# Optimization experiments

Measured on AMD Instinct MI355X. Metric: run time of the kernel, lower is better.

Reference implementation:

```python
import jax, jax.numpy as jnp
import numpy as np

B, T, C, H, DH = 2, 2048, 768, 12, 64


def setup_inputs() -> dict:
    key = jax.random.key(0)
    k1, k2, k3 = jax.random.split(key, 3)
    x = jax.random.normal(k1, (B, T, C), dtype=jnp.float32)
    Wqkv = jax.random.normal(k2, (C, 3 * C), dtype=jnp.float32) * (C ** -0.5)
    Wout = jax.random.normal(k3, (C, C), dtype=jnp.float32) * (C ** -0.5)
    return {"x": x, "Wqkv": Wqkv, "Wout": Wout}


def reference(x, Wqkv, Wout):
    b, t, c = x.shape
    qkv = x @ Wqkv  # [B,T,3C]
    q, k, v = jnp.split(qkv, 3, axis=-1)
    # [B,T,C] -> [B,H,T,dh]
    q = q.reshape(b, t, H, DH).transpose(0, 2, 1, 3)
    k = k.reshape(b, t, H, DH).transpose(0, 2, 1, 3)
    v = v.reshape(b, t, H, DH).transpose(0, 2, 1, 3)
    scale = DH ** -0.5
    scores = jnp.einsum('bhqd,bhkd->bhqk', q, k) * scale  # [B,H,T,T]
    causal = jnp.tril(jnp.ones((t, t), dtype=bool))
    scores = jnp.where(causal, scores, -jnp.inf)
    weights = jax.nn.softmax(scores, axis=-1)
    # dropout p=0.0 -> identity
    out = jnp.einsum('bhqk,bhkd->bhqd', weights, v)  # [B,H,T,dh]
    out = out.transpose(0, 2, 1, 3).reshape(b, t, c)
    return out @ Wout
```

## Files before the change

### kernel.cpp

```cpp
#include <hip/hip_runtime.h>
#include <hip/hip_bf16.h>

#define Bn 2
#define Tn 2048
#define Cn 768
#define Hn 12
#define Dn 64
#define N3n 2304
#define Mn 4096

#define MASKVAL (-30000.f)
#define NIT_G 144
#define DEFER_THR 64.f
#define L2E8 0.1803368801111204f

typedef unsigned short u16;
typedef __attribute__((ext_vector_type(8))) unsigned short ushort8_t;
typedef __attribute__((ext_vector_type(8))) short bf16x8;
typedef __attribute__((ext_vector_type(4))) float f32x4;
typedef __attribute__((ext_vector_type(2))) unsigned int uint2v;
typedef __attribute__((address_space(1))) unsigned int* gas1_t;
typedef __attribute__((address_space(3))) unsigned int* las3_t;

__device__ __forceinline__ float bf2f(u16 u) {
  union { unsigned int i; float f; } v; v.i = ((unsigned int)u) << 16; return v.f;
}
__device__ __forceinline__ u16 f2bf(float f) {
  union { float f; unsigned int i; } v; v.f = f;
  return (u16)((v.i + 0x7fffu + ((v.i >> 16) & 1u)) >> 16);
}

#define E(qt, s0, s1, ck) (((qt) << 24) | ((s0) << 16) | ((s1) << 8) | (ck))
__constant__ unsigned int SCHED[48] = {
    E(31, 0, 8, 0), E(31, 8, 16, 1), E(30, 0, 8, 0), E(30, 8, 16, 1),
    E(29, 0, 8, 0), E(28, 0, 8, 0), E(15, 0, 8, 2), E(14, 0, 8, 2),
    E(29, 8, 15, 1), E(28, 8, 15, 1), E(27, 0, 7, 0), E(27, 7, 14, 1),
    E(26, 0, 7, 0), E(26, 7, 14, 1), E(25, 0, 7, 0), E(24, 0, 7, 0),
    E(13, 0, 7, 2), E(12, 0, 7, 2),
    E(25, 7, 13, 1), E(24, 7, 13, 1), E(23, 0, 6, 0), E(23, 6, 12, 1),
    E(22, 0, 6, 0), E(22, 6, 12, 1), E(21, 0, 6, 0), E(20, 0, 6, 0),
    E(11, 0, 6, 2), E(10, 0, 6, 2),
    E(21, 6, 11, 1), E(20, 6, 11, 1), E(19, 0, 5, 0), E(19, 5, 10, 1),
    E(18, 0, 5, 0), E(18, 5, 10, 1), E(17, 0, 5, 0), E(16, 0, 5, 0),
    E(9, 0, 5, 2), E(8, 0, 5, 2),
    E(17, 5, 9, 1), E(16, 5, 9, 1), E(7, 0, 4, 2), E(6, 0, 4, 2),
    E(5, 0, 3, 2), E(4, 0, 3, 2), E(3, 0, 2, 2), E(2, 0, 2, 2),
    E(1, 0, 1, 2), E(0, 0, 1, 2)};

__global__ __launch_bounds__(256) void prep_kernel(const float* __restrict__ x,
                                                   const float* __restrict__ Wqkv,
                                                   const float* __restrict__ Wout,
                                                   u16* __restrict__ xb,
                                                   u16* __restrict__ WqkvT,
                                                   u16* __restrict__ WoutT,
                                                   int* __restrict__ counter) {
  __shared__ u16 t[32][33];
  const int bx = blockIdx.x;
  const int tid = threadIdx.x;
  if (bx < 3072) {
    if (bx == 0 && tid < 8) counter[tid] = 0;
    const int i = (bx * 256 + tid) * 4;
    float4 v = *(const float4*)(x + i);
    ushort4 s;
    s.x = f2bf(v.x); s.y = f2bf(v.y); s.z = f2bf(v.z); s.w = f2bf(v.w);
    *(ushort4*)(xb + i) = s;
  } else {
    const int idx = bx - 3072;
    const int gx = idx % 96, gy = idx / 96;
    const bool isA = gx < (N3n / 32);
    const float* in = isA ? Wqkv : Wout;
    u16* out = isA ? WqkvT : WoutT;
    const int Cc = isA ? N3n : Cn;
    const int c0 = (isA ? gx : gx - N3n / 32) * 32;
    const int r0 = gy * 32;
    const int tx = tid & 31, ty = tid >> 5;
#pragma unroll
    for (int i = 0; i < 4; i++)
      t[ty * 4 + i][tx] = f2bf(in[(size_t)(r0 + ty * 4 + i) * Cc + c0 + tx]);
    __syncthreads();
#pragma unroll
    for (int i = 0; i < 4; i++)
      out[(size_t)(c0 + ty * 4 + i) * Cn + r0 + tx] = t[tx][ty * 4 + i];
  }
}

#define BK 64
#define GT_W (128 * BK)

template <int EPI>
__global__ __launch_bounds__(256) void mfma_gemm(const u16* __restrict__ A,
                                                 const u16* __restrict__ BT,
                                                 u16* __restrict__ Q,
                                                 u16* __restrict__ Kd,
                                                 u16* __restrict__ VT,
                                                 float* __restrict__ out) {
  __shared__ __align__(16) u16 Ash[2 * GT_W];
  __shared__ __align__(16) u16 Bsh[2 * GT_W];
  const int tid = threadIdx.x;
  const int wv = tid >> 6, lane = tid & 63;
  const int lo = lane & 15, quad = lane >> 4;
  const int lo7 = lo & 7;
  const int wm = wv & 1, wn = wv >> 1;

  const int nwg = gridDim.x * gridDim.y;
  const int cpx = nwg >> 3;
  const int lid = blockIdx.y * gridDim.x + blockIdx.x;
  const int swz = (lid & 7) * cpx + (lid >> 3);
  const int n0 = (swz % gridDim.x) * 128;
  const int m0 = (swz / gridDim.x) * 128;

  const int srow = lane >> 3;
  const int kcol = ((lane & 7) ^ srow) << 3;

  f32x4 acc[4][4];
#pragma unroll
  for (int i = 0; i < 4; i++)
#pragma unroll
    for (int j = 0; j < 4; j++) acc[i][j] = f32x4{0.f, 0.f, 0.f, 0.f};

  auto stage = [&](int k0, int buf) {
#pragma unroll
    for (int c = 0; c < 4; c++) {
      const int rb = (wv << 5) + (c << 3);
      const int gr = rb + srow;
      __builtin_amdgcn_global_load_lds(
          (gas1_t)(A + (size_t)(m0 + gr) * Cn + k0 + kcol),
          (las3_t)(&Ash[buf * GT_W + rb * BK]), 16, 0, 0);
      __builtin_amdgcn_global_load_lds(
          (gas1_t)(BT + (size_t)(n0 + gr) * Cn + k0 + kcol),
          (las3_t)(&Bsh[buf * GT_W + rb * BK]), 16, 0, 0);
    }
  };

  stage(0, 0);
  __syncthreads();

  int cur = 0;
  for (int k0 = 0; k0 < Cn; k0 += BK) {
    if (k0 + BK < Cn) stage(k0 + BK, cur ^ 1);

    const u16* Ab = &Ash[cur * GT_W];
    const u16* Bb = &Bsh[cur * GT_W];
    bf16x8 af[4][2], bfr[4][2];
#pragma unroll
    for (int t = 0; t < 4; t++) {
#pragma unroll
      for (int s = 0; s < 2; s++) {
        const int cc = ((s * 4 + quad) ^ lo7) << 3;
        af[t][s]  = *(const bf16x8*)&Ab[(wm * 64 + t * 16 + lo) * BK + cc];
        bfr[t][s] = *(const bf16x8*)&Bb[(wn * 64 + t * 16 + lo) * BK + cc];
      }
    }
#pragma unroll
    for (int mt = 0; mt < 4; mt++)
#pragma unroll
      for (int nt = 0; nt < 4; nt++) {
        acc[mt][nt] = __builtin_amdgcn_mfma_f32_16x16x32_bf16(af[mt][0], bfr[nt][0],
                                                              acc[mt][nt], 0, 0, 0);
        acc[mt][nt] = __builtin_amdgcn_mfma_f32_16x16x32_bf16(af[mt][1], bfr[nt][1],
                                                              acc[mt][nt], 0, 0, 0);
      }
    __syncthreads();
    cur ^= 1;
  }

  if (EPI == 0) {
    const int which = n0 / Cn;
    const int h = ((n0 % Cn) >> 6) + wn;
    const int bb = m0 >> 11;
    const int t_base = (m0 & (Tn - 1)) + wm * 64;
    if (which < 2) {
      u16* dst = ((which == 0) ? Q : Kd) + (size_t)(bb * Hn + h) * Tn * Dn;
#pragma unroll
      for (int mt = 0; mt < 4; mt++)
#pragma unroll
        for (int nt = 0; nt < 4; nt++)
#pragma unroll
          for (int r = 0; r < 4; r++) {
            const int t = t_base + mt * 16 + (quad << 2) + r;
            dst[(size_t)t * Dn + nt * 16 + lo] = f2bf(acc[mt][nt][r]);
          }
    } else {
      u16* dst = VT + (size_t)(bb * Hn + h) * Dn * Tn;
#pragma unroll
      for (int mt = 0; mt < 4; mt++)
#pragma unroll
        for (int nt = 0; nt < 4; nt++) {
          const int t = t_base + mt * 16 + (quad << 2);
          const int d = nt * 16 + lo;
          ushort4 st;
          st.x = f2bf(acc[mt][nt][0]); st.y = f2bf(acc[mt][nt][1]);
          st.z = f2bf(acc[mt][nt][2]); st.w = f2bf(acc[mt][nt][3]);
          *(ushort4*)&dst[(size_t)d * Tn + t] = st;
        }
    }
  } else {
#pragma unroll
    for (int mt = 0; mt < 4; mt++)
#pragma unroll
      for (int nt = 0; nt < 4; nt++)
#pragma unroll
        for (int r = 0; r < 4; r++) {
          const int m = m0 + wm * 64 + mt * 16 + (quad << 2) + r;
          out[(size_t)m * Cn + n0 + wn * 64 + nt * 16 + lo] = acc[mt][nt][r];
        }
  }
}

#define KT_W (128 * 64)
#define VH_W (64 * 64)

__global__ __launch_bounds__(256) void attn_kernel(const u16* __restrict__ Q,
                                                   const u16* __restrict__ K,
                                                   const u16* __restrict__ VT,
                                                   u16* __restrict__ O,
                                                   int* __restrict__ counter,
                                                   float* __restrict__ po,
                                                   float* __restrict__ pm,
                                                   float* __restrict__ pl) {
  __shared__ __align__(16) u16 Ksh[2 * KT_W];
  __shared__ __align__(16) u16 Vsh[4 * VH_W];
  int* sip = (int*)&Ksh[KT_W];

  const int tid = threadIdx.x;
  const int g = blockIdx.x & 7;
  const int wv = tid >> 6, lane = tid & 63;
  const int lo = lane & 15, quad = lane >> 4;
  const int lo7 = lo & 7;
  const int ck0 = (quad ^ lo7) << 3;
  const int ck1 = ck0 ^ 32;
  const int sr = tid >> 3;
  const int sc = (tid & 7) << 3;
  const int kcol = ((lane & 7) ^ (lane >> 3)) << 3;
  const int t7 = tid & 7;
  const int vb0 = (((t7 & 6) ^ (sr & 7)) << 3) + ((t7 & 1) << 2);
  const int vb1 = ((((t7 & 6) | 1) ^ (sr & 7)) << 3) + ((t7 & 1) << 2);

  for (;;) {
    if (tid == 0) *sip = atomicAdd(&counter[g], 1);
    __syncthreads();
    const int il = *sip;
    if (il >= NIT_G) return;

    const unsigned int e = SCHED[il / 3];
    const int qt = e >> 24, ck = e & 255;
    const int jstart = ((e >> 16) & 255) << 7;
    const int jend   = ((e >> 8) & 255) << 7;
    const int q0 = qt << 6;
    const int hb = g * 3 + il % 3;
    const int h = hb % 12, b = hb / 12;
    const size_t base = (size_t)(b * Hn + h) * Tn * Dn;
    const size_t vtb  = (size_t)(b * Hn + h) * Dn * Tn;
    const u16* Kg = K + base;

    const u16* qp = Q + base + (size_t)(q0 + (wv << 4) + lo) * Dn + (quad << 3);
    const bf16x8 aq0 = *(const bf16x8*)qp;
    const bf16x8 aq1 = *(const bf16x8*)(qp + 32);

    f32x4 o[4] = {f32x4{0,0,0,0}, f32x4{0,0,0,0}, f32x4{0,0,0,0}, f32x4{0,0,0,0}};
    float m1 = MASKVAL;
    float l1 = 0.f;

#pragma unroll
    for (int c = 0; c < 4; c++) {
      const int rb = (wv << 5) + (c << 3);
      __builtin_amdgcn_global_load_lds(
          (gas1_t)(Kg + (size_t)(jstart + rb + (lane >> 3)) * Dn + kcol),
          (las3_t)(&Ksh[rb * 64]), 16, 0, 0);
    }
#pragma unroll
    for (int hf = 0; hf < 2; hf++)
#pragma unroll
      for (int it = 0; it < 2; it++) {
        const int r = sr + it * 32;
        union { ushort8_t u; uint2v hh[2]; } vv;
        vv.u = *(const ushort8_t*)(VT + vtb + (size_t)r * Tn + jstart + hf * 64 + sc);
        *(uint2v*)&Vsh[hf * VH_W + r * 64 + vb0] = vv.hh[0];
        *(uint2v*)&Vsh[hf * VH_W + r * 64 + vb1] = vv.hh[1];
      }
    __syncthreads();

    int cur = 0;
    const int qg = q0 + (wv << 4) + lo;

    for (int j0 = jstart; j0 < jend; j0 += 128) {
      const bool hasnext = (j0 + 128 < jend);

      ushort8_t vr[4];
      if (hasnext) {
        const int nb = cur ^ 1;
#pragma unroll
        for (int c = 0; c < 4; c++) {
          const int rb = (wv << 5) + (c << 3);
          __builtin_amdgcn_global_load_lds(
              (gas1_t)(Kg + (size_t)(j0 + 128 + rb + (lane >> 3)) * Dn + kcol),
              (las3_t)(&Ksh[nb * KT_W + rb * 64]), 16, 0, 0);
        }
#pragma unroll
        for (int hf = 0; hf < 2; hf++)
#pragma unroll
          for (int it = 0; it < 2; it++) {
            const int r = sr + it * 32;
            vr[hf * 2 + it] =
                *(const ushort8_t*)(VT + vtb + (size_t)r * Tn + j0 + 128 + hf * 64 + sc);
          }
      }

      const u16* Kb_ = &Ksh[cur * KT_W];
      const u16* VbA = &Vsh[cur * 2 * VH_W];
      const u16* VbB = VbA + VH_W;

      f32x4 s[8];
      __builtin_amdgcn_s_setprio(1);
#pragma unroll
      for (int nt = 0; nt < 8; nt++) {
        const bf16x8 bk0 = *(const bf16x8*)(&Kb_[(nt * 16 + lo) * 64 + ck0]);
        const bf16x8 bk1 = *(const bf16x8*)(&Kb_[(nt * 16 + lo) * 64 + ck1]);
        f32x4 a = {0.f, 0.f, 0.f, 0.f};
        a = __builtin_amdgcn_mfma_f32_16x16x32_bf16(bk0, aq0, a, 0, 0, 0);
        a = __builtin_amdgcn_mfma_f32_16x16x32_bf16(bk1, aq1, a, 0, 0, 0);
        s[nt] = a;
      }
      __builtin_amdgcn_s_setprio(0);

      if (j0 + 128 > q0) {
#pragma unroll
        for (int nt = 0; nt < 8; nt++)
#pragma unroll
          for (int r = 0; r < 4; r++) {
            const int kvg = j0 + nt * 16 + (quad << 2) + r;
            if (kvg > qg) s[nt][r] = MASKVAL;
          }
      }

      float gm[8];
#pragma unroll
      for (int nt = 0; nt < 8; nt++)
        gm[nt] = fmaxf(fmaxf(s[nt][0], s[nt][1]), fmaxf(s[nt][2], s[nt][3]));
      const float pmax = fmaxf(fmaxf(fmaxf(gm[0], gm[1]), fmaxf(gm[2], gm[3])),
                               fmaxf(fmaxf(gm[4], gm[5]), fmaxf(gm[6], gm[7])));

      if (!__all(pmax <= m1 + DEFER_THR)) {
        float mr = fmaxf(pmax, __shfl_xor(pmax, 16));
        mr = fmaxf(mr, __shfl_xor(mr, 32));
        const float mnew = fmaxf(m1, mr);
        const float alpha = __builtin_amdgcn_exp2f(L2E8 * (m1 - mnew));
        m1 = mnew;
        l1 *= alpha;
        float ar[4];
#pragma unroll
        for (int r = 0; r < 4; r++) ar[r] = __shfl(alpha, (quad << 2) + r);
#pragma unroll
        for (int nt = 0; nt < 4; nt++)
#pragma unroll
          for (int r = 0; r < 4; r++) o[nt][r] *= ar[r];
      }

      const float mb2 = L2E8 * m1;
#pragma unroll
      for (int nt = 0; nt < 8; nt++)
#pragma unroll
        for (int r = 0; r < 4; r++)
          s[nt][r] = __builtin_amdgcn_exp2f(L2E8 * s[nt][r] - mb2);
      {
        float gs[8];
#pragma unroll
        for (int nt = 0; nt < 8; nt++)
          gs[nt] = (s[nt][0] + s[nt][1]) + (s[nt][2] + s[nt][3]);
        l1 += ((gs[0] + gs[1]) + (gs[2] + gs[3])) +
              ((gs[4] + gs[5]) + (gs[6] + gs[7]));
      }

      unsigned int A0, B0, A1, B1, A2, B2, A3, B3;
      union { unsigned int w[4]; bf16x8 v; } pa0u, pa1u, pa2u, pa3u;
      asm("v_cvt_pk_bf16_f32 %0, %1, %2" : "=v"(A0) : "v"(s[0][0]), "v"(s[0][1]));
      asm("v_cvt_pk_bf16_f32 %0, %1, %2" : "=v"(B0) : "v"(s[0][2]), "v"(s[0][3]));
      asm("v_cvt_pk_bf16_f32 %0, %1, %2" : "=v"(A1) : "v"(s[1][0]), "v"(s[1][1]));
      asm("v_cvt_pk_bf16_f32 %0, %1, %2" : "=v"(B1) : "v"(s[1][2]), "v"(s[1][3]));
      asm("v_cvt_pk_bf16_f32 %0, %1, %2" : "=v"(A2) : "v"(s[2][0]), "v"(s[2][1]));
      asm("v_cvt_pk_bf16_f32 %0, %1, %2" : "=v"(B2) : "v"(s[2][2]), "v"(s[2][3]));
      asm("v_cvt_pk_bf16_f32 %0, %1, %2" : "=v"(A3) : "v"(s[3][0]), "v"(s[3][1]));
      asm("v_cvt_pk_bf16_f32 %0, %1, %2" : "=v"(B3) : "v"(s[3][2]), "v"(s[3][3]));
      {
        const auto rA01 = __builtin_amdgcn_permlane32_swap(A0, A1, false, false);
        const auto rB01 = __builtin_amdgcn_permlane32_swap(B0, B1, false, false);
        const auto rA23 = __builtin_amdgcn_permlane32_swap(A2, A3, false, false);
        const auto rB23 = __builtin_amdgcn_permlane32_swap(B2, B3, false, false);
        pa0u.w[0] = rA01[0]; pa0u.w[1] = rB01[0];
        pa0u.w[2] = rA01[1]; pa0u.w[3] = rB01[1];
        pa1u.w[0] = rA23[0]; pa1u.w[1] = rB23[0];
        pa1u.w[2] = rA23[1]; pa1u.w[3] = rB23[1];
      }
      asm("v_cvt_pk_bf16_f32 %0, %1, %2" : "=v"(A0) : "v"(s[4][0]), "v"(s[4][1]));
      asm("v_cvt_pk_bf16_f32 %0, %1, %2" : "=v"(B0) : "v"(s[4][2]), "v"(s[4][3]));
      asm("v_cvt_pk_bf16_f32 %0, %1, %2" : "=v"(A1) : "v"(s[5][0]), "v"(s[5][1]));
      asm("v_cvt_pk_bf16_f32 %0, %1, %2" : "=v"(B1) : "v"(s[5][2]), "v"(s[5][3]));
      asm("v_cvt_pk_bf16_f32 %0, %1, %2" : "=v"(A2) : "v"(s[6][0]), "v"(s[6][1]));
      asm("v_cvt_pk_bf16_f32 %0, %1, %2" : "=v"(B2) : "v"(s[6][2]), "v"(s[6][3]));
      asm("v_cvt_pk_bf16_f32 %0, %1, %2" : "=v"(A3) : "v"(s[7][0]), "v"(s[7][1]));
      asm("v_cvt_pk_bf16_f32 %0, %1, %2" : "=v"(B3) : "v"(s[7][2]), "v"(s[7][3]));
      {
        const auto rA01 = __builtin_amdgcn_permlane32_swap(A0, A1, false, false);
        const auto rB01 = __builtin_amdgcn_permlane32_swap(B0, B1, false, false);
        const auto rA23 = __builtin_amdgcn_permlane32_swap(A2, A3, false, false);
        const auto rB23 = __builtin_amdgcn_permlane32_swap(B2, B3, false, false);
        pa2u.w[0] = rA01[0]; pa2u.w[1] = rB01[0];
        pa2u.w[2] = rA01[1]; pa2u.w[3] = rB01[1];
        pa3u.w[0] = rA23[0]; pa3u.w[1] = rB23[0];
        pa3u.w[2] = rA23[1]; pa3u.w[3] = rB23[1];
      }

      __builtin_amdgcn_s_setprio(1);
#pragma unroll
      for (int nt = 0; nt < 4; nt++) {
        const bf16x8 bvA0 = *(const bf16x8*)(&VbA[(nt * 16 + lo) * 64 + ck0]);
        const bf16x8 bvA1 = *(const bf16x8*)(&VbA[(nt * 16 + lo) * 64 + ck1]);
        const bf16x8 bvB0 = *(const bf16x8*)(&VbB[(nt * 16 + lo) * 64 + ck0]);
        const bf16x8 bvB1 = *(const bf16x8*)(&VbB[(nt * 16 + lo) * 64 + ck1]);
        o[nt] = __builtin_amdgcn_mfma_f32_16x16x32_bf16(pa0u.v, bvA0, o[nt], 0, 0, 0);
        o[nt] = __builtin_amdgcn_mfma_f32_16x16x32_bf16(pa1u.v, bvA1, o[nt], 0, 0, 0);
        o[nt] = __builtin_amdgcn_mfma_f32_16x16x32_bf16(pa2u.v, bvB0, o[nt], 0, 0, 0);
        o[nt] = __builtin_amdgcn_mfma_f32_16x16x32_bf16(pa3u.v, bvB1, o[nt], 0, 0, 0);
      }
      __builtin_amdgcn_s_setprio(0);

      if (hasnext) {
        const int nb = cur ^ 1;
#pragma unroll
        for (int hf = 0; hf < 2; hf++)
#pragma unroll
          for (int it = 0; it < 2; it++) {
            const int r = sr + it * 32;
            union { ushort8_t u; uint2v hh[2]; } vv;
            vv.u = vr[hf * 2 + it];
            *(uint2v*)&Vsh[nb * 2 * VH_W + hf * VH_W + r * 64 + vb0] = vv.hh[0];
            *(uint2v*)&Vsh[nb * 2 * VH_W + hf * VH_W + r * 64 + vb1] = vv.hh[1];
          }
      }
      __syncthreads();
      cur ^= 1;
    }

    float lt = l1;
    lt += __shfl_xor(lt, 16);
    lt += __shfl_xor(lt, 32);
    const float linv = 1.f / lt;
    float ir[4];
#pragma unroll
    for (int r = 0; r < 4; r++) ir[r] = __shfl(linv, (quad << 2) + r);

    if (ck == 2) {
#pragma unroll
      for (int nt = 0; nt < 4; nt++)
#pragma unroll
        for (int r = 0; r < 4; r++) {
          const int row = q0 + (wv << 4) + (quad << 2) + r;
          const int col = h * 64 + nt * 16 + lo;
          O[(size_t)(b * Tn + row) * Cn + col] = f2bf(o[nt][r] * ir[r]);
        }
    } else {
      const int st = hb * 16 + (qt - 16);
      const int pidx = st * 2 + ck;
      float* pO = po + ((size_t)pidx << 12);
#pragma unroll
      for (int nt = 0; nt < 4; nt++)
#pragma unroll
        for (int r = 0; r < 4; r++)
          pO[((wv << 4) + (quad << 2) + r) * 64 + nt * 16 + lo] = o[nt][r] * ir[r];
      if (quad == 0) {
        pm[pidx * 64 + (wv << 4) + lo] = m1;
        pl[pidx * 64 + (wv << 4) + lo] = lt;
      }
    }
  }
}

__global__ __launch_bounds__(256) void combine_kernel(const float* __restrict__ po,
                                                      const float* __restrict__ pm,
                                                      const float* __restrict__ pl,
                                                      u16* __restrict__ O) {
  const int st = blockIdx.x;
  const int hb = st >> 4;
  const int h = hb % 12, b = hb / 12;
  const int q0 = (16 + (st & 15)) << 6;
  const int tid = threadIdx.x;
  const int row = tid >> 2, cc0 = (tid & 3) << 4;
  const float* pa = po + (((size_t)st * 2) << 12) + row * 64 + cc0;
  const float* pb = pa + 4096;
  const float ma = pm[st * 128 + row],      la = pl[st * 128 + row];
  const float mb = pm[st * 128 + 64 + row], lb = pl[st * 128 + 64 + row];
  const float mm = fmaxf(ma, mb);
  float wa = la * __builtin_amdgcn_exp2f(L2E8 * (ma - mm));
  float wb = lb * __builtin_amdgcn_exp2f(L2E8 * (mb - mm));
  const float wi = 1.f / (wa + wb);
  wa *= wi; wb *= wi;
  u16* Orow = O + (size_t)(b * Tn + q0 + row) * Cn + h * 64 + cc0;
#pragma unroll
  for (int i = 0; i < 16; i += 4) {
    const float4 va = *(const float4*)(pa + i);
    const float4 vb = *(const float4*)(pb + i);
    ushort4 s4;
    s4.x = f2bf(wa * va.x + wb * vb.x);
    s4.y = f2bf(wa * va.y + wb * vb.y);
    s4.z = f2bf(wa * va.z + wb * vb.z);
    s4.w = f2bf(wa * va.w + wb * vb.w);
    *(ushort4*)(Orow + i) = s4;
  }
}

extern "C" void kernel_launch(void* const* d_in, const int* in_sizes, int n_in,
                              void* d_out, int out_size, void* d_ws, size_t ws_size,
                              hipStream_t stream) {
  const float* x    = (const float*)d_in[0];
  const float* Wqkv = (const float*)d_in[1];
  const float* Wout = (const float*)d_in[2];
  float* out = (float*)d_out;

  const size_t per = (size_t)Bn * Hn * Tn * Dn;
  u16* xb    = (u16*)d_ws;
  u16* WqkvT = xb + (size_t)Mn * Cn;
  u16* WoutT = WqkvT + (size_t)N3n * Cn;
  u16* Qb    = WoutT + (size_t)Cn * Cn;
  u16* Kb    = Qb + per;
  u16* VTb   = Kb + per;
  u16* attn  = VTb + per;
  int* counter = (int*)(attn + (size_t)Mn * Cn);
  float* po = (float*)(counter + 512);
  float* pm = po + (size_t)768 * 4096;
  float* pl = pm + (size_t)768 * 64;

  prep_kernel<<<dim3(3072 + 2304), 256, 0, stream>>>(x, Wqkv, Wout, xb, WqkvT,
                                                     WoutT, counter);
  mfma_gemm<0><<<dim3(N3n / 128, Mn / 128), 256, 0, stream>>>(xb, WqkvT, Qb, Kb, VTb, nullptr);
  attn_kernel<<<dim3(512), 256, 0, stream>>>(Qb, Kb, VTb, attn, counter, po, pm, pl);
  combine_kernel<<<dim3(384), 256, 0, stream>>>(po, pm, pl, attn);
  mfma_gemm<1><<<dim3(Cn / 128, Mn / 128), 256, 0, stream>>>(attn, WoutT, nullptr, nullptr, nullptr, out);
}
```

Measured before the change: 166.4 us.

## Drop split-KV partitioning and combine kernel; process each query tile fully

Replaces the schedule that split long causal query tiles into two KV chunks with a simple longest-first list of whole tiles. Every attention work item now writes bf16 output directly, and the partial-result buffers and separate combine kernel are removed. This saves a kernel launch and the fp32 partial traffic through global memory. The cost is coarser, more uneven work items that can lengthen the tail of the persistent scheduler.

Measured after the change: 158.3 us. -4.8%, faster.

```diff
diff --git a/kernel.cpp b/kernel.cpp
--- a/kernel.cpp
+++ b/kernel.cpp
@@ -10,7 +10,7 @@
 #define Mn 4096
 
 #define MASKVAL (-30000.f)
-#define NIT_G 144
+#define NIT_G 96
 #define DEFER_THR 64.f
 #define L2E8 0.1803368801111204f
 
@@ -30,22 +30,14 @@
   return (u16)((v.i + 0x7fffu + ((v.i >> 16) & 1u)) >> 16);
 }
 
-#define E(qt, s0, s1, ck) (((qt) << 24) | ((s0) << 16) | ((s1) << 8) | (ck))
-__constant__ unsigned int SCHED[48] = {
-    E(31, 0, 8, 0), E(31, 8, 16, 1), E(30, 0, 8, 0), E(30, 8, 16, 1),
-    E(29, 0, 8, 0), E(28, 0, 8, 0), E(15, 0, 8, 2), E(14, 0, 8, 2),
-    E(29, 8, 15, 1), E(28, 8, 15, 1), E(27, 0, 7, 0), E(27, 7, 14, 1),
-    E(26, 0, 7, 0), E(26, 7, 14, 1), E(25, 0, 7, 0), E(24, 0, 7, 0),
-    E(13, 0, 7, 2), E(12, 0, 7, 2),
-    E(25, 7, 13, 1), E(24, 7, 13, 1), E(23, 0, 6, 0), E(23, 6, 12, 1),
-    E(22, 0, 6, 0), E(22, 6, 12, 1), E(21, 0, 6, 0), E(20, 0, 6, 0),
-    E(11, 0, 6, 2), E(10, 0, 6, 2),
-    E(21, 6, 11, 1), E(20, 6, 11, 1), E(19, 0, 5, 0), E(19, 5, 10, 1),
-    E(18, 0, 5, 0), E(18, 5, 10, 1), E(17, 0, 5, 0), E(16, 0, 5, 0),
-    E(9, 0, 5, 2), E(8, 0, 5, 2),
-    E(17, 5, 9, 1), E(16, 5, 9, 1), E(7, 0, 4, 2), E(6, 0, 4, 2),
-    E(5, 0, 3, 2), E(4, 0, 3, 2), E(3, 0, 2, 2), E(2, 0, 2, 2),
-    E(1, 0, 1, 2), E(0, 0, 1, 2)};
+#define E(qt, L) (((qt) << 8) | (L))
+__constant__ unsigned int SCHED[32] = {
+    E(31, 16), E(30, 16), E(29, 15), E(28, 15), E(27, 14), E(26, 14),
+    E(25, 13), E(24, 13), E(23, 12), E(22, 12), E(21, 11), E(20, 11),
+    E(19, 10), E(18, 10), E(17, 9),  E(16, 9),  E(15, 8),  E(14, 8),
+    E(13, 7),  E(12, 7),  E(11, 6),  E(10, 6),  E(9, 5),   E(8, 5),
+    E(7, 4),   E(6, 4),   E(5, 3),   E(4, 3),   E(3, 2),   E(2, 2),
+    E(1, 1),   E(0, 1)};
 
 __global__ __launch_bounds__(256) void prep_kernel(const float* __restrict__ x,
                                                    const float* __restrict__ Wqkv,
@@ -214,10 +206,7 @@
                                                    const u16* __restrict__ K,
                                                    const u16* __restrict__ VT,
                                                    u16* __restrict__ O,
-                                                   int* __restrict__ counter,
-                                                   float* __restrict__ po,
-                                                   float* __restrict__ pm,
-                                                   float* __restrict__ pl) {
+                                                   int* __restrict__ counter) {
   __shared__ __align__(16) u16 Ksh[2 * KT_W];
   __shared__ __align__(16) u16 Vsh[4 * VH_W];
   int* sip = (int*)&Ksh[KT_W];
@@ -243,9 +232,8 @@
     if (il >= NIT_G) return;
 
     const unsigned int e = SCHED[il / 3];
-    const int qt = e >> 24, ck = e & 255;
-    const int jstart = ((e >> 16) & 255) << 7;
-    const int jend   = ((e >> 8) & 255) << 7;
+    const int qt = e >> 8;
+    const int jend = (e & 255) << 7;
     const int q0 = qt << 6;
     const int hb = g * 3 + il % 3;
     const int h = hb % 12, b = hb / 12;
@@ -265,7 +253,7 @@
     for (int c = 0; c < 4; c++) {
       const int rb = (wv << 5) + (c << 3);
       __builtin_amdgcn_global_load_lds(
-          (gas1_t)(Kg + (size_t)(jstart + rb + (lane >> 3)) * Dn + kcol),
+          (gas1_t)(Kg + (size_t)(rb + (lane >> 3)) * Dn + kcol),
           (las3_t)(&Ksh[rb * 64]), 16, 0, 0);
     }
 #pragma unroll
@@ -274,7 +262,7 @@
       for (int it = 0; it < 2; it++) {
         const int r = sr + it * 32;
         union { ushort8_t u; uint2v hh[2]; } vv;
-        vv.u = *(const ushort8_t*)(VT + vtb + (size_t)r * Tn + jstart + hf * 64 + sc);
+        vv.u = *(const ushort8_t*)(VT + vtb + (size_t)r * Tn + hf * 64 + sc);
         *(uint2v*)&Vsh[hf * VH_W + r * 64 + vb0] = vv.hh[0];
         *(uint2v*)&Vsh[hf * VH_W + r * 64 + vb1] = vv.hh[1];
       }
@@ -283,7 +271,7 @@
     int cur = 0;
     const int qg = q0 + (wv << 4) + lo;
 
-    for (int j0 = jstart; j0 < jend; j0 += 128) {
+    for (int j0 = 0; j0 < jend; j0 += 128) {
       const bool hasnext = (j0 + 128 < jend);
 
       ushort8_t vr[4];
@@ -449,62 +437,14 @@
 #pragma unroll
     for (int r = 0; r < 4; r++) ir[r] = __shfl(linv, (quad << 2) + r);
 
-    if (ck == 2) {
-#pragma unroll
-      for (int nt = 0; nt < 4; nt++)
-#pragma unroll
-        for (int r = 0; r < 4; r++) {
-          const int row = q0 + (wv << 4) + (quad << 2) + r;
-          const int col = h * 64 + nt * 16 + lo;
-          O[(size_t)(b * Tn + row) * Cn + col] = f2bf(o[nt][r] * ir[r]);
-        }
-    } else {
-      const int st = hb * 16 + (qt - 16);
-      const int pidx = st * 2 + ck;
-      float* pO = po + ((size_t)pidx << 12);
-#pragma unroll
-      for (int nt = 0; nt < 4; nt++)
-#pragma unroll
-        for (int r = 0; r < 4; r++)
-          pO[((wv << 4) + (quad << 2) + r) * 64 + nt * 16 + lo] = o[nt][r] * ir[r];
-      if (quad == 0) {
-        pm[pidx * 64 + (wv << 4) + lo] = m1;
-        pl[pidx * 64 + (wv << 4) + lo] = lt;
-      }
-    }
-  }
-}
-
-__global__ __launch_bounds__(256) void combine_kernel(const float* __restrict__ po,
-                                                      const float* __restrict__ pm,
-                                                      const float* __restrict__ pl,
-                                                      u16* __restrict__ O) {
-  const int st = blockIdx.x;
-  const int hb = st >> 4;
-  const int h = hb % 12, b = hb / 12;
-  const int q0 = (16 + (st & 15)) << 6;
-  const int tid = threadIdx.x;
-  const int row = tid >> 2, cc0 = (tid & 3) << 4;
-  const float* pa = po + (((size_t)st * 2) << 12) + row * 64 + cc0;
-  const float* pb = pa + 4096;
-  const float ma = pm[st * 128 + row],      la = pl[st * 128 + row];
-  const float mb = pm[st * 128 + 64 + row], lb = pl[st * 128 + 64 + row];
-  const float mm = fmaxf(ma, mb);
-  float wa = la * __builtin_amdgcn_exp2f(L2E8 * (ma - mm));
-  float wb = lb * __builtin_amdgcn_exp2f(L2E8 * (mb - mm));
-  const float wi = 1.f / (wa + wb);
-  wa *= wi; wb *= wi;
-  u16* Orow = O + (size_t)(b * Tn + q0 + row) * Cn + h * 64 + cc0;
-#pragma unroll
-  for (int i = 0; i < 16; i += 4) {
-    const float4 va = *(const float4*)(pa + i);
-    const float4 vb = *(const float4*)(pb + i);
-    ushort4 s4;
-    s4.x = f2bf(wa * va.x + wb * vb.x);
-    s4.y = f2bf(wa * va.y + wb * vb.y);
-    s4.z = f2bf(wa * va.z + wb * vb.z);
-    s4.w = f2bf(wa * va.w + wb * vb.w);
-    *(ushort4*)(Orow + i) = s4;
+#pragma unroll
+    for (int nt = 0; nt < 4; nt++)
+#pragma unroll
+      for (int r = 0; r < 4; r++) {
+        const int row = q0 + (wv << 4) + (quad << 2) + r;
+        const int col = h * 64 + nt * 16 + lo;
+        O[(size_t)(b * Tn + row) * Cn + col] = f2bf(o[nt][r] * ir[r]);
+      }
   }
 }
 
@@ -525,14 +465,10 @@
   u16* VTb   = Kb + per;
   u16* attn  = VTb + per;
   int* counter = (int*)(attn + (size_t)Mn * Cn);
-  float* po = (float*)(counter + 512);
-  float* pm = po + (size_t)768 * 4096;
-  float* pl = pm + (size_t)768 * 64;
 
   prep_kernel<<<dim3(3072 + 2304), 256, 0, stream>>>(x, Wqkv, Wout, xb, WqkvT,
                                                      WoutT, counter);
   mfma_gemm<0><<<dim3(N3n / 128, Mn / 128), 256, 0, stream>>>(xb, WqkvT, Qb, Kb, VTb, nullptr);
-  attn_kernel<<<dim3(512), 256, 0, stream>>>(Qb, Kb, VTb, attn, counter, po, pm, pl);
-  combine_kernel<<<dim3(384), 256, 0, stream>>>(po, pm, pl, attn);
+  attn_kernel<<<dim3(512), 256, 0, stream>>>(Qb, Kb, VTb, attn, counter);
   mfma_gemm<1><<<dim3(Cn / 128, Mn / 128), 256, 0, stream>>>(attn, WoutT, nullptr, nullptr, nullptr, out);
 }
```
